# Kernel tuning notes

Hardware: AMD Instinct MI355X
Metric: run time of the kernel (lower is better)

Reference implementation:

```python
import jax, jax.numpy as jnp
import numpy as np

T, N, E, C = 16, 20000, 320000, 128
EPS = 1e-5


def setup_inputs() -> dict:
    key = jax.random.key(0)
    ks = jax.random.split(key, 6)
    x = jax.random.normal(ks[0], (T, N, C), dtype=jnp.float32)
    edge_index = jax.random.randint(ks[1], (2, E), 0, N, dtype=jnp.int32)
    edge_weight = jax.random.uniform(ks[2], (E,), dtype=jnp.float32)
    # temporal Conv1d weight [out, in, k=3], scaled like torch default init
    Wt = jax.random.normal(ks[3], (C, C, 3), dtype=jnp.float32) * (1.0 / np.sqrt(C * 3))
    bt = jnp.zeros((C,), dtype=jnp.float32)
    # GCNConv linear weight [out, in] (no bias) + separate aggregation bias
    Wg = jax.random.normal(ks[4], (C, C), dtype=jnp.float32) * (1.0 / np.sqrt(C))
    bg = jnp.zeros((C,), dtype=jnp.float32)
    gamma = jnp.ones((C,), dtype=jnp.float32)
    beta = jnp.zeros((C,), dtype=jnp.float32)
    return {"x": x, "edge_index": edge_index, "edge_weight": edge_weight,
            "Wt": Wt, "bt": bt, "Wg": Wg, "bg": bg, "gamma": gamma, "beta": beta}


def _forward(x, edge_index, edge_weight, Wt, bt, Wg, bg, gamma, beta):
    # temporal conv: treat nodes as batch -> [N, C, T]
    xc = jnp.transpose(x, (1, 2, 0))
    h = jax.lax.conv_general_dilated(xc, Wt, window_strides=(1,),
                                     padding=[(1, 1)],
                                     dimension_numbers=("NCH", "OIH", "NCH"))
    h = h + bt[None, :, None]
    h = jnp.transpose(h, (2, 0, 1))  # [T, N, C]

    # GCN normalization with self-loops (fill_value=1.0)
    loops = jnp.arange(N, dtype=edge_index.dtype)
    src = jnp.concatenate([edge_index[0], loops])
    dst = jnp.concatenate([edge_index[1], loops])
    w = jnp.concatenate([edge_weight, jnp.ones((N,), edge_weight.dtype)])
    deg = jax.ops.segment_sum(w, dst, num_segments=N)
    dinv = jnp.where(deg > 0, jax.lax.rsqrt(jnp.maximum(deg, 1e-12)), 0.0)
    norm = dinv[src] * w * dinv[dst]  # [E+N]

    def step(carry, x_t):
        ht = x_t @ Wg.T                                 # [N, C]
        msg = ht[src] * norm[:, None]                   # [E+N, C]
        agg = jax.ops.segment_sum(msg, dst, num_segments=N) + bg
        mu = agg.mean(axis=0)
        var = jnp.mean((agg - mu) ** 2, axis=0)         # biased, training BN
        y = gamma * (agg - mu) * jax.lax.rsqrt(var + EPS) + beta
        return carry, jax.nn.relu(y)

    _, out = jax.lax.scan(step, None, h)  # [T, N, C]
    return out


def reference(x, edge_index, edge_weight, Wt, bt, Wg, bg, gamma, beta):
    return _forward(x, edge_index, edge_weight, Wt, bt, Wg, bg, gamma, beta)
```

## Files before the change

kernel.cpp:

```cpp
#include <hip/hip_runtime.h>
#include <cstdint>

#define TT 16
#define NN 20000
#define CC 128
#define EE 320000
#define KKDIM 384
#define EPSV 1e-5f
#define SBLK 512
#define SCAT_BLKS 1329
#define CAST_BLKS 1280

typedef unsigned short u16;
typedef u16 u16x4 __attribute__((ext_vector_type(4)));
typedef u16 u16x8 __attribute__((ext_vector_type(8)));
typedef __bf16 bf16x8 __attribute__((ext_vector_type(8)));
typedef float f32x4 __attribute__((ext_vector_type(4)));

static __device__ __forceinline__ u16 f2bf(float f) {
  union { float f; uint32_t u; } v; v.f = f;
  uint32_t u = v.u;
  return (u16)((u + 0x7FFFu + ((u >> 16) & 1u)) >> 16);
}
static __device__ __forceinline__ float bf2f(u16 h) {
  union { uint32_t u; float f; } v; v.u = ((uint32_t)h) << 16;
  return v.f;
}
static __device__ __forceinline__ uint32_t cvtpk(float lo, float hi) {
  uint32_t r;
  asm volatile("v_cvt_pk_bf16_f32 %0, %1, %2" : "=v"(r) : "v"(lo), "v"(hi));
  return r;
}

__global__ __launch_bounds__(384) void k_prep(const float* __restrict__ Wt,
                                              const float* __restrict__ bt,
                                              const float* __restrict__ Wg,
                                              u16* __restrict__ BmatT,
                                              float* __restrict__ b2,
                                              const int* __restrict__ ei,
                                              const float* __restrict__ ew,
                                              float* __restrict__ deg,
                                              int* __restrict__ cnt) {
  const int b = blockIdx.x;
  if (b < 128) {
    const int o = b;
    const int kk = threadIdx.x;
    const int k = kk >> 7, i = kk & 127;
    float acc = 0.f;
    for (int c = 0; c < CC; ++c)
      acc += Wg[o * CC + c] * Wt[(size_t)c * 384 + i * 3 + k];
    BmatT[(size_t)o * KKDIM + kk] = f2bf(acc);
    if (kk == 0) {
      float bb = 0.f;
      for (int c = 0; c < CC; ++c) bb += Wg[o * CC + c] * bt[c];
      b2[o] = bb;
    }
  } else {
    int e = (b - 128) * 384 + threadIdx.x;
    if (e < EE) {
      int d = ei[EE + e];
      atomicAdd(&deg[d], ew[e]);
      atomicAdd(&cnt[d], 1);
    }
  }
}

__global__ __launch_bounds__(1024) void k_scan(const int* __restrict__ cnt,
                                               float* __restrict__ deg,
                                               int* __restrict__ rowptr) {
  __shared__ int part[1024];
  const int tid = threadIdx.x;
  const int base = tid * 20;
  int s = 0;
  for (int j = 0; j < 20; ++j) {
    int idx = base + j;
    if (idx < NN) {
      s += cnt[idx] + 1;
      deg[idx] = rsqrtf(deg[idx] + 1.0f);
    }
  }
  part[tid] = s;
  __syncthreads();
  for (int off = 1; off < 1024; off <<= 1) {
    int u = 0;
    if (tid >= off) u = part[tid - off];
    __syncthreads();
    part[tid] += u;
    __syncthreads();
  }
  int run = part[tid] - s;
  for (int j = 0; j < 20; ++j) {
    int idx = base + j;
    if (idx < NN) { rowptr[idx] = run; run += cnt[idx] + 1; }
  }
  if (tid == 1023) rowptr[NN] = part[1023];
}

__global__ __launch_bounds__(256) void k_scatter(const int* __restrict__ ei,
                                                 const float* __restrict__ ew,
                                                 const int* __restrict__ rowptr,
                                                 int* __restrict__ fill,
                                                 const float* __restrict__ dinv,
                                                 int2* __restrict__ cw,
                                                 const float* __restrict__ x,
                                                 u16* __restrict__ xb) {
  const int b = blockIdx.x;
  if (b < SCAT_BLKS) {
    int e = b * 256 + threadIdx.x;
    if (e < EE) {
      int s = ei[e], d = ei[EE + e];
      int pos = rowptr[d] + atomicAdd(&fill[d], 1);
      cw[pos] = make_int2(s, __float_as_int(dinv[s] * ew[e] * dinv[d]));
    } else if (e < EE + NN) {
      int n = e - EE;
      float dn = dinv[n];
      int pos = rowptr[n] + atomicAdd(&fill[n], 1);
      cw[pos] = make_int2(n, __float_as_int(dn * dn));
    }
  } else {
    const int cb = b - SCAT_BLKS;
    const size_t tot = (size_t)TT * NN * CC;
    const size_t stride = (size_t)CAST_BLKS * 256 * 8;
    for (size_t i = ((size_t)cb * 256 + threadIdx.x) * 8; i < tot; i += stride) {
      float4 v0 = *(const float4*)(x + i);
      float4 v1 = *(const float4*)(x + i + 4);
      uint32_t p0 = cvtpk(v0.x, v0.y);
      uint32_t p1 = cvtpk(v0.z, v0.w);
      uint32_t p2 = cvtpk(v1.x, v1.y);
      uint32_t p3 = cvtpk(v1.z, v1.w);
      uint32_t* dst = (uint32_t*)(xb + i);
      dst[0] = p0; dst[1] = p1; dst[2] = p2; dst[3] = p3;
    }
  }
}

__global__ __launch_bounds__(256) void k_conv(const u16* __restrict__ xb,
                                              const u16* __restrict__ BmatT,
                                              const float* __restrict__ b2,
                                              u16* __restrict__ ht) {
  const int bid = blockIdx.x;
  const int xcd = bid & 7;
  const int s = bid >> 3;
  const int tile = xcd * 20 + (s % 20);
  const int t = s / 20;
  if (tile >= 157) return;
  __shared__ __align__(16) u16 As[128][72];
  __shared__ __align__(16) u16 Bs[128][72];
  const int row0 = tile * 128;
  const int tid = threadIdx.x;
  const int lane = tid & 63;
  const int wv = tid >> 6;

  f32x4 acc[2][8];
  for (int m = 0; m < 2; ++m)
    for (int nb = 0; nb < 8; ++nb) acc[m][nb] = (f32x4){0.f, 0.f, 0.f, 0.f};

  for (int kt = 0; kt < 6; ++kt) {
    const int kTap = kt >> 1;
    const int i0 = (kt & 1) * 64;
    const int tk = t + kTap - 1;
    const bool tkv = (tk >= 0) && (tk < TT);
    #pragma unroll
    for (int j = 0; j < 4; ++j) {
      const int idx = tid + j * 256;
      const int r = idx >> 3;
      const int q = idx & 7;
      u16x8 v = (u16x8){0, 0, 0, 0, 0, 0, 0, 0};
      if (tkv && row0 + r < NN)
        v = *(const u16x8*)(xb + ((size_t)tk * NN + row0 + r) * CC + i0 + q * 8);
      *(u16x8*)&As[r][q * 8] = v;
    }
    #pragma unroll
    for (int j = 0; j < 4; ++j) {
      const int idx = tid + j * 256;
      const int col = idx >> 3, q = idx & 7;
      *(u16x8*)&Bs[col][q * 8] =
          *(const u16x8*)(BmatT + (size_t)col * KKDIM + kt * 64 + q * 8);
    }
    __syncthreads();
    #pragma unroll
    for (int ks = 0; ks < 2; ++ks) {
      const int k0 = ks * 32 + ((lane >> 4) << 3);
      bf16x8 a0 = __builtin_bit_cast(bf16x8, *(const u16x8*)&As[wv * 32 + (lane & 15)][k0]);
      bf16x8 a1 = __builtin_bit_cast(bf16x8, *(const u16x8*)&As[wv * 32 + 16 + (lane & 15)][k0]);
      #pragma unroll
      for (int nb = 0; nb < 8; ++nb) {
        bf16x8 b = __builtin_bit_cast(bf16x8, *(const u16x8*)&Bs[nb * 16 + (lane & 15)][k0]);
        acc[0][nb] = __builtin_amdgcn_mfma_f32_16x16x32_bf16(a0, b, acc[0][nb], 0, 0, 0);
        acc[1][nb] = __builtin_amdgcn_mfma_f32_16x16x32_bf16(a1, b, acc[1][nb], 0, 0, 0);
      }
    }
    __syncthreads();
  }
  float b2v[8];
  #pragma unroll
  for (int nb = 0; nb < 8; ++nb) b2v[nb] = b2[nb * 16 + (lane & 15)];
  const int rb = row0 + wv * 32 + ((lane >> 4) << 2);
  #pragma unroll
  for (int m = 0; m < 2; ++m)
    #pragma unroll
    for (int nb = 0; nb < 8; ++nb)
      #pragma unroll
      for (int j = 0; j < 4; ++j) {
        const int r = rb + m * 16 + j;
        if (r < NN)
          ht[(size_t)r * 2048 + t * 128 + nb * 16 + (lane & 15)] =
              f2bf(acc[m][nb][j] + b2v[nb]);
      }
}

__global__ __launch_bounds__(256) void k_agg(const u16* __restrict__ ht,
                                             const int2* __restrict__ cw,
                                             const int* __restrict__ rowptr,
                                             u16* __restrict__ agg) {
  const int bid = blockIdx.x;
  const int tg = bid & 7;
  const int wv = threadIdx.x >> 6, lane = threadIdx.x & 63;
  const int n = (bid >> 3) * 4 + wv;
  const int o0 = tg * 256 + lane * 4;
  float acc[4] = {0.f, 0.f, 0.f, 0.f};
  const int beg = rowptr[n], end = rowptr[n + 1];
  int p = beg;
  for (; p + 8 <= end; p += 8) {
    int2 e0 = cw[p],     e1 = cw[p + 1], e2 = cw[p + 2], e3 = cw[p + 3];
    int2 e4 = cw[p + 4], e5 = cw[p + 5], e6 = cw[p + 6], e7 = cw[p + 7];
    u16x4 v0 = *(const u16x4*)(ht + (size_t)e0.x * 2048 + o0);
    u16x4 v1 = *(const u16x4*)(ht + (size_t)e1.x * 2048 + o0);
    u16x4 v2 = *(const u16x4*)(ht + (size_t)e2.x * 2048 + o0);
    u16x4 v3 = *(const u16x4*)(ht + (size_t)e3.x * 2048 + o0);
    u16x4 v4 = *(const u16x4*)(ht + (size_t)e4.x * 2048 + o0);
    u16x4 v5 = *(const u16x4*)(ht + (size_t)e5.x * 2048 + o0);
    u16x4 v6 = *(const u16x4*)(ht + (size_t)e6.x * 2048 + o0);
    u16x4 v7 = *(const u16x4*)(ht + (size_t)e7.x * 2048 + o0);
    #define ACC1(e_, v_)                                              \
      {                                                               \
        const float w_ = __int_as_float((e_).y);                      \
        _Pragma("unroll") for (int k = 0; k < 4; ++k)                 \
            acc[k] = fmaf(bf2f((v_)[k]), w_, acc[k]);                 \
      }
    ACC1(e0, v0) ACC1(e1, v1) ACC1(e2, v2) ACC1(e3, v3)
    ACC1(e4, v4) ACC1(e5, v5) ACC1(e6, v6) ACC1(e7, v7)
  }
  for (; p < end; ++p) {
    int2 e = cw[p];
    u16x4 v = *(const u16x4*)(ht + (size_t)e.x * 2048 + o0);
    ACC1(e, v)
  }
  #undef ACC1
  u16x4 sv;
  #pragma unroll
  for (int k = 0; k < 4; ++k) sv[k] = f2bf(acc[k]);
  *(u16x4*)(agg + (size_t)n * 2048 + o0) = sv;
}

__global__ __launch_bounds__(256) void k_stats(const u16* __restrict__ agg,
                                               float* __restrict__ partial) {
  const int tid = threadIdx.x;
  const int t = tid >> 4, seg = tid & 15;
  const int c0 = seg * 8;
  float s[8], q[8];
  #pragma unroll
  for (int j = 0; j < 8; ++j) { s[j] = 0.f; q[j] = 0.f; }
  const int nbeg = blockIdx.x * 40;
  const int nend = (nbeg + 40 < NN) ? nbeg + 40 : NN;
  for (int n = nbeg; n < nend; ++n) {
    u16x8 v = *(const u16x8*)(agg + (size_t)n * 2048 + t * 128 + c0);
    #pragma unroll
    for (int j = 0; j < 8; ++j) {
      float f = bf2f(v[j]);
      s[j] += f; q[j] += f * f;
    }
  }
  float* dst = partial + (size_t)blockIdx.x * 4096;
  #pragma unroll
  for (int j = 0; j < 8; ++j) {
    dst[t * 256 + c0 + j] = s[j];
    dst[t * 256 + 128 + c0 + j] = q[j];
  }
}

__global__ __launch_bounds__(256) void k_fin(const float* __restrict__ partial,
                                             const float* __restrict__ gamma,
                                             const float* __restrict__ beta,
                                             float* __restrict__ scsh) {
  __shared__ float red[256];
  __shared__ float vals[32];
  const int blk = blockIdx.x;
  const int t = blk >> 3;
  const int cbase = (blk & 7) * 16;
  const int tid = threadIdx.x;
  const int tcl = tid & 31;
  const int bt = tid >> 5;
  const int tcv = t * 256 + ((tcl < 16) ? (cbase + tcl) : (128 + cbase + tcl - 16));
  float s = 0.f;
  #pragma unroll 8
  for (int k = 0; k < 64; ++k)
    s += partial[(size_t)(bt + (k << 3)) * 4096 + tcv];
  red[tid] = s;
  __syncthreads();
  if (tid < 32) {
    float tot = 0.f;
    #pragma unroll
    for (int i = 0; i < 8; ++i) tot += red[i * 32 + tid];
    vals[tid] = tot;
  }
  __syncthreads();
  if (tid < 16) {
    const int c = cbase + tid;
    float su = vals[tid], sq = vals[16 + tid];
    const float inv_n = 1.f / (float)NN;
    float mu = su * inv_n;
    float var = sq * inv_n - mu * mu;
    float sc = gamma[c] * rsqrtf(var + EPSV);
    scsh[t * 256 + c] = sc;
    scsh[t * 256 + 128 + c] = beta[c] - sc * mu;
  }
}

__global__ __launch_bounds__(256) void k_norm(const u16* __restrict__ agg,
                                              const float* __restrict__ scsh,
                                              float* __restrict__ out) {
  const int n = blockIdx.x;
  const int t = threadIdx.x >> 4, seg = threadIdx.x & 15;
  const int c0 = seg * 8;
  u16x8 v = *(const u16x8*)(agg + (size_t)n * 2048 + t * 128 + c0);
  float4 sc0 = *(const float4*)(scsh + t * 256 + c0);
  float4 sc1 = *(const float4*)(scsh + t * 256 + c0 + 4);
  float4 sh0 = *(const float4*)(scsh + t * 256 + 128 + c0);
  float4 sh1 = *(const float4*)(scsh + t * 256 + 128 + c0 + 4);
  f32x4 r0, r1;
  r0[0] = fmaxf(fmaf(bf2f(v[0]), sc0.x, sh0.x), 0.f);
  r0[1] = fmaxf(fmaf(bf2f(v[1]), sc0.y, sh0.y), 0.f);
  r0[2] = fmaxf(fmaf(bf2f(v[2]), sc0.z, sh0.z), 0.f);
  r0[3] = fmaxf(fmaf(bf2f(v[3]), sc0.w, sh0.w), 0.f);
  r1[0] = fmaxf(fmaf(bf2f(v[4]), sc1.x, sh1.x), 0.f);
  r1[1] = fmaxf(fmaf(bf2f(v[5]), sc1.y, sh1.y), 0.f);
  r1[2] = fmaxf(fmaf(bf2f(v[6]), sc1.z, sh1.z), 0.f);
  r1[3] = fmaxf(fmaf(bf2f(v[7]), sc1.w, sh1.w), 0.f);
  float* dst = out + (size_t)t * (NN * CC) + (size_t)n * CC + c0;
  __builtin_nontemporal_store(r0, (f32x4*)dst);
  __builtin_nontemporal_store(r1, (f32x4*)(dst + 4));
}

extern "C" void kernel_launch(void* const* d_in, const int* in_sizes, int n_in,
                              void* d_out, int out_size, void* d_ws, size_t ws_size,
                              hipStream_t stream) {
  const float* x     = (const float*)d_in[0];
  const int*   ei    = (const int*)d_in[1];
  const float* ew    = (const float*)d_in[2];
  const float* Wt    = (const float*)d_in[3];
  const float* bt    = (const float*)d_in[4];
  const float* Wg    = (const float*)d_in[5];
  const float* gamma = (const float*)d_in[7];
  const float* beta  = (const float*)d_in[8];
  float* out = (float*)d_out;
  char* ws = (char*)d_ws;

  const size_t off_cnt    = 0;
  const size_t off_fill   = 80000;
  const size_t off_deg    = 176384;
  const size_t zero_bytes = 256384;
  const size_t off_rowptr = 256384;
  const size_t off_cw     = 336400;
  const size_t off_BmatT  = 3056400;
  const size_t off_b2     = 3154704;
  const size_t off_scsh   = 3155216;
  const size_t off_ht     = 3171600;
  const size_t off_agg    = 85091600;

  int*   cnt    = (int*)(ws + off_cnt);
  int*   fill   = (int*)(ws + off_fill);
  float* deg    = (float*)(ws + off_deg);
  int*   rowptr = (int*)(ws + off_rowptr);
  int2*  cw     = (int2*)(ws + off_cw);
  u16*   BmatT  = (u16*)(ws + off_BmatT);
  float* b2     = (float*)(ws + off_b2);
  float* scsh   = (float*)(ws + off_scsh);
  u16*   ht     = (u16*)(ws + off_ht);
  u16*   agg    = (u16*)(ws + off_agg);
  u16*   xb     = (u16*)(ws + off_agg);
  float* partial = (float*)(ws + off_ht);

  hipMemsetAsync(ws, 0, zero_bytes, stream);
  k_prep<<<dim3(128 + (EE + 383) / 384), dim3(384), 0, stream>>>(
      Wt, bt, Wg, BmatT, b2, ei, ew, deg, cnt);
  k_scan<<<dim3(1), dim3(1024), 0, stream>>>(cnt, deg, rowptr);
  k_scatter<<<dim3(SCAT_BLKS + CAST_BLKS), dim3(256), 0, stream>>>(
      ei, ew, rowptr, fill, deg, cw, x, xb);
  k_conv<<<dim3(2560), dim3(256), 0, stream>>>(xb, BmatT, b2, ht);
  k_agg<<<dim3(40000), dim3(256), 0, stream>>>(ht, cw, rowptr, agg);
  k_stats<<<dim3(SBLK), dim3(256), 0, stream>>>(agg, partial);
  k_fin<<<dim3(128), dim3(256), 0, stream>>>(partial, gamma, beta, scsh);
  k_norm<<<dim3(NN), dim3(256), 0, stream>>>(agg, scsh, out);
}
```

Before: 493.2 us.

## Load conv tiles via global_load_lds with XOR swizzle; move fp32→bf16 cast into prep

The conv GEMM now fills its LDS tiles with direct global-to-LDS 16-byte loads instead of going through registers. The tiles use an unpadded layout with an XOR swizzle to avoid bank conflicts, and out-of-range rows are clamped to the last valid row rather than zeroed. Separately, the fp32-to-bf16 cast of x moves from the scatter kernel into the prep kernel, so it overlaps with the degree-count atomics instead of the CSR scatter. The new load path depends on the global_load_lds builtin writing each lane's data at the expected LDS addresses. The clamped rows feed only output rows that are never stored.

After: 456.9 us (median of 2 runs). 7.4% less time.

```diff
diff --git a/kernel.cpp b/kernel.cpp
--- a/kernel.cpp
+++ b/kernel.cpp
@@ -8,7 +8,7 @@
 #define KKDIM 384
 #define EPSV 1e-5f
 #define SBLK 512
-#define SCAT_BLKS 1329
+#define PREP_EDGE_BLKS 834
 #define CAST_BLKS 1280
 
 typedef unsigned short u16;
@@ -16,6 +16,11 @@
 typedef u16 u16x8 __attribute__((ext_vector_type(8)));
 typedef __bf16 bf16x8 __attribute__((ext_vector_type(8)));
 typedef float f32x4 __attribute__((ext_vector_type(4)));
+
+#define GLOAD_LDS16(g_, l_)                                              \
+  __builtin_amdgcn_global_load_lds(                                      \
+      (const __attribute__((address_space(1))) unsigned int*)(g_),       \
+      (__attribute__((address_space(3))) unsigned int*)(l_), 16, 0, 0)
 
 static __device__ __forceinline__ u16 f2bf(float f) {
   union { float f; uint32_t u; } v; v.f = f;
@@ -40,7 +45,9 @@
                                               const int* __restrict__ ei,
                                               const float* __restrict__ ew,
                                               float* __restrict__ deg,
-                                              int* __restrict__ cnt) {
+                                              int* __restrict__ cnt,
+                                              const float* __restrict__ x,
+                                              u16* __restrict__ xb) {
   const int b = blockIdx.x;
   if (b < 128) {
     const int o = b;
@@ -55,12 +62,26 @@
       for (int c = 0; c < CC; ++c) bb += Wg[o * CC + c] * bt[c];
       b2[o] = bb;
     }
-  } else {
+  } else if (b < 128 + PREP_EDGE_BLKS) {
     int e = (b - 128) * 384 + threadIdx.x;
     if (e < EE) {
       int d = ei[EE + e];
       atomicAdd(&deg[d], ew[e]);
       atomicAdd(&cnt[d], 1);
+    }
+  } else {
+    const int cb = b - 128 - PREP_EDGE_BLKS;
+    const size_t tot = (size_t)TT * NN * CC;
+    const size_t stride = (size_t)CAST_BLKS * 384 * 8;
+    for (size_t i = ((size_t)cb * 384 + threadIdx.x) * 8; i < tot; i += stride) {
+      float4 v0 = *(const float4*)(x + i);
+      float4 v1 = *(const float4*)(x + i + 4);
+      uint32_t p0 = cvtpk(v0.x, v0.y);
+      uint32_t p1 = cvtpk(v0.z, v0.w);
+      uint32_t p2 = cvtpk(v1.x, v1.y);
+      uint32_t p3 = cvtpk(v1.z, v1.w);
+      uint32_t* dst = (uint32_t*)(xb + i);
+      dst[0] = p0; dst[1] = p1; dst[2] = p2; dst[3] = p3;
     }
   }
 }
@@ -101,36 +122,17 @@
                                                  const int* __restrict__ rowptr,
                                                  int* __restrict__ fill,
                                                  const float* __restrict__ dinv,
-                                                 int2* __restrict__ cw,
-                                                 const float* __restrict__ x,
-                                                 u16* __restrict__ xb) {
-  const int b = blockIdx.x;
-  if (b < SCAT_BLKS) {
-    int e = b * 256 + threadIdx.x;
-    if (e < EE) {
-      int s = ei[e], d = ei[EE + e];
-      int pos = rowptr[d] + atomicAdd(&fill[d], 1);
-      cw[pos] = make_int2(s, __float_as_int(dinv[s] * ew[e] * dinv[d]));
-    } else if (e < EE + NN) {
-      int n = e - EE;
-      float dn = dinv[n];
-      int pos = rowptr[n] + atomicAdd(&fill[n], 1);
-      cw[pos] = make_int2(n, __float_as_int(dn * dn));
-    }
-  } else {
-    const int cb = b - SCAT_BLKS;
-    const size_t tot = (size_t)TT * NN * CC;
-    const size_t stride = (size_t)CAST_BLKS * 256 * 8;
-    for (size_t i = ((size_t)cb * 256 + threadIdx.x) * 8; i < tot; i += stride) {
-      float4 v0 = *(const float4*)(x + i);
-      float4 v1 = *(const float4*)(x + i + 4);
-      uint32_t p0 = cvtpk(v0.x, v0.y);
-      uint32_t p1 = cvtpk(v0.z, v0.w);
-      uint32_t p2 = cvtpk(v1.x, v1.y);
-      uint32_t p3 = cvtpk(v1.z, v1.w);
-      uint32_t* dst = (uint32_t*)(xb + i);
-      dst[0] = p0; dst[1] = p1; dst[2] = p2; dst[3] = p3;
-    }
+                                                 int2* __restrict__ cw) {
+  int e = blockIdx.x * 256 + threadIdx.x;
+  if (e < EE) {
+    int s = ei[e], d = ei[EE + e];
+    int pos = rowptr[d] + atomicAdd(&fill[d], 1);
+    cw[pos] = make_int2(s, __float_as_int(dinv[s] * ew[e] * dinv[d]));
+  } else if (e < EE + NN) {
+    int n = e - EE;
+    float dn = dinv[n];
+    int pos = rowptr[n] + atomicAdd(&fill[n], 1);
+    cw[pos] = make_int2(n, __float_as_int(dn * dn));
   }
 }
 
@@ -144,8 +146,8 @@
   const int tile = xcd * 20 + (s % 20);
   const int t = s / 20;
   if (tile >= 157) return;
-  __shared__ __align__(16) u16 As[128][72];
-  __shared__ __align__(16) u16 Bs[128][72];
+  __shared__ __align__(16) u16 As[8192];
+  __shared__ __align__(16) u16 Bs[8192];
   const int row0 = tile * 128;
   const int tid = threadIdx.x;
   const int lane = tid & 63;
@@ -161,31 +163,45 @@
     const int tk = t + kTap - 1;
     const bool tkv = (tk >= 0) && (tk < TT);
     #pragma unroll
-    for (int j = 0; j < 4; ++j) {
-      const int idx = tid + j * 256;
-      const int r = idx >> 3;
-      const int q = idx & 7;
-      u16x8 v = (u16x8){0, 0, 0, 0, 0, 0, 0, 0};
-      if (tkv && row0 + r < NN)
-        v = *(const u16x8*)(xb + ((size_t)tk * NN + row0 + r) * CC + i0 + q * 8);
-      *(u16x8*)&As[r][q * 8] = v;
-    }
-    #pragma unroll
-    for (int j = 0; j < 4; ++j) {
-      const int idx = tid + j * 256;
-      const int col = idx >> 3, q = idx & 7;
-      *(u16x8*)&Bs[col][q * 8] =
-          *(const u16x8*)(BmatT + (size_t)col * KKDIM + kt * 64 + q * 8);
+    for (int k = 0; k < 4; ++k) {
+      const int Lb = wv * 256 + k * 64;
+      const int L = Lb + lane;
+      const int col = L >> 3, q = L & 7;
+      const u16* src = BmatT + (size_t)col * KKDIM + kt * 64 + ((q ^ (col & 7)) << 3);
+      GLOAD_LDS16(src, &Bs[Lb * 8]);
+    }
+    if (tkv) {
+      #pragma unroll
+      for (int k = 0; k < 4; ++k) {
+        const int Lb = wv * 256 + k * 64;
+        const int L = Lb + lane;
+        const int r = L >> 3, q = L & 7;
+        const int grow = (row0 + r < NN) ? (row0 + r) : (NN - 1);
+        const u16* src = xb + ((size_t)tk * NN + grow) * CC + i0 + ((q ^ (r & 7)) << 3);
+        GLOAD_LDS16(src, &As[Lb * 8]);
+      }
+    } else {
+      #pragma unroll
+      for (int k = 0; k < 4; ++k) {
+        const int L = wv * 256 + k * 64 + lane;
+        *(u16x8*)&As[L * 8] = (u16x8){0, 0, 0, 0, 0, 0, 0, 0};
+      }
     }
     __syncthreads();
     #pragma unroll
     for (int ks = 0; ks < 2; ++ks) {
-      const int k0 = ks * 32 + ((lane >> 4) << 3);
-      bf16x8 a0 = __builtin_bit_cast(bf16x8, *(const u16x8*)&As[wv * 32 + (lane & 15)][k0]);
-      bf16x8 a1 = __builtin_bit_cast(bf16x8, *(const u16x8*)&As[wv * 32 + 16 + (lane & 15)][k0]);
+      const int kq = ks * 4 + (lane >> 4);
+      const int ar0 = wv * 32 + (lane & 15);
+      const int ar1 = ar0 + 16;
+      bf16x8 a0 = __builtin_bit_cast(bf16x8,
+          *(const u16x8*)&As[ar0 * 64 + ((kq ^ (ar0 & 7)) << 3)]);
+      bf16x8 a1 = __builtin_bit_cast(bf16x8,
+          *(const u16x8*)&As[ar1 * 64 + ((kq ^ (ar1 & 7)) << 3)]);
       #pragma unroll
       for (int nb = 0; nb < 8; ++nb) {
-        bf16x8 b = __builtin_bit_cast(bf16x8, *(const u16x8*)&Bs[nb * 16 + (lane & 15)][k0]);
+        const int col = nb * 16 + (lane & 15);
+        bf16x8 b = __builtin_bit_cast(bf16x8,
+            *(const u16x8*)&Bs[col * 64 + ((kq ^ (col & 7)) << 3)]);
         acc[0][nb] = __builtin_amdgcn_mfma_f32_16x16x32_bf16(a0, b, acc[0][nb], 0, 0, 0);
         acc[1][nb] = __builtin_amdgcn_mfma_f32_16x16x32_bf16(a1, b, acc[1][nb], 0, 0, 0);
       }
@@ -382,11 +398,11 @@
   float* partial = (float*)(ws + off_ht);
 
   hipMemsetAsync(ws, 0, zero_bytes, stream);
-  k_prep<<<dim3(128 + (EE + 383) / 384), dim3(384), 0, stream>>>(
-      Wt, bt, Wg, BmatT, b2, ei, ew, deg, cnt);
+  k_prep<<<dim3(128 + PREP_EDGE_BLKS + CAST_BLKS), dim3(384), 0, stream>>>(
+      Wt, bt, Wg, BmatT, b2, ei, ew, deg, cnt, x, xb);
   k_scan<<<dim3(1), dim3(1024), 0, stream>>>(cnt, deg, rowptr);
-  k_scatter<<<dim3(SCAT_BLKS + CAST_BLKS), dim3(256), 0, stream>>>(
-      ei, ew, rowptr, fill, deg, cw, x, xb);
+  k_scatter<<<dim3((EE + NN + 255) / 256), dim3(256), 0, stream>>>(ei, ew, rowptr,
+                                                                   fill, deg, cw);
   k_conv<<<dim3(2560), dim3(256), 0, stream>>>(xb, BmatT, b2, ht);
   k_agg<<<dim3(40000), dim3(256), 0, stream>>>(ht, cw, rowptr, agg);
   k_stats<<<dim3(SBLK), dim3(256), 0, stream>>>(agg, partial);
```
